# Performance work log

Hardware: AMD Instinct MI355X
Metric: run time of the kernel (lower is better)

The kernel has to match this reference:

```python
import jax, jax.numpy as jnp
import numpy as np

H, W = 256, 512
SCORE_THR = 0.2
NMS_THR = 0.15
TOPK = 4096


def _make_anchors():
    xs = (np.arange(W) + 0.5) * 0.4 - 0.2 * W
    ys = (np.arange(H) + 0.5) * 0.4 - 0.2 * H
    gx, gy = np.meshgrid(xs, ys)            # [H, W]
    anc = np.zeros((H, W, 2, 7), dtype=np.float32)
    anc[..., 0] = gx[..., None]
    anc[..., 1] = gy[..., None]
    anc[..., 2] = -1.0
    anc[..., 3] = 1.56  # h
    anc[..., 4] = 1.6   # w
    anc[..., 5] = 3.9   # l
    anc[..., 0, 6] = 0.0
    anc[..., 1, 6] = np.pi / 2
    return jnp.asarray(anc)


def _make_T(theta, tx, ty, tz):
    c, s = np.cos(theta), np.sin(theta)
    T = np.eye(4, dtype=np.float32)
    T[0, 0], T[0, 1], T[1, 0], T[1, 1] = c, -s, s, c
    T[0, 3], T[1, 3], T[2, 3] = tx, ty, tz
    return jnp.asarray(T)


def setup_inputs() -> dict:
    key = jax.random.key(0)
    k1, k2, k3, k4 = jax.random.split(key, 4)
    return {
        "anchors": _make_anchors(),
        "psm_v": jax.random.normal(k1, (1, 2, H, W), jnp.float32),
        "rm_v": jax.random.normal(k2, (1, 14, H, W), jnp.float32) * 0.1,
        "psm_i": jax.random.normal(k3, (1, 2, H, W), jnp.float32),
        "rm_i": jax.random.normal(k4, (1, 14, H, W), jnp.float32) * 0.1,
        "t_proj": _make_T(0.05, 2.0, -1.0, 0.1),
        "t_ego": _make_T(-0.1, 5.0, 3.0, 0.0),
    }


def delta_to_boxes3d(rm, anchors):
    # rm: [1, 14, H, W] -> [A, 7]; anchors: [H, W, 2, 7] xyzhwlr -> [A, 7]
    d = jnp.transpose(rm[0], (1, 2, 0)).reshape(-1, 7)
    a = anchors.reshape(-1, 7)
    ad = jnp.sqrt(a[:, 4] ** 2 + a[:, 5] ** 2)          # diag of w,l
    xy = d[:, :2] * ad[:, None] + a[:, :2]
    z = d[:, 2] * a[:, 3] + a[:, 2]
    dims = jnp.exp(d[:, 3:6]) * a[:, 3:6]               # h, w, l
    yaw = d[:, 6] + a[:, 6]
    return jnp.concatenate([xy, z[:, None], dims, yaw[:, None]], axis=1)


def boxes_to_corners_3d(b):
    # b: [N, 7] x,y,z,h,w,l,yaw (order 'hwl') -> [N, 8, 3]
    h, w, l, yaw = b[:, 3], b[:, 4], b[:, 5], b[:, 6]
    sx = jnp.array([1, 1, -1, -1, 1, 1, -1, -1], jnp.float32) * 0.5
    sy = jnp.array([1, -1, -1, 1, 1, -1, -1, 1], jnp.float32) * 0.5
    sz = jnp.array([-1, -1, -1, -1, 1, 1, 1, 1], jnp.float32) * 0.5
    x = l[:, None] * sx
    y = w[:, None] * sy
    z = h[:, None] * sz
    c, s = jnp.cos(yaw)[:, None], jnp.sin(yaw)[:, None]
    xr = x * c - y * s + b[:, 0:1]
    yr = x * s + y * c + b[:, 1:2]
    zr = z + b[:, 2:3]
    return jnp.stack([xr, yr, zr], axis=-1)


def project_box3d(corners, T):
    # corners: [N, 8, 3]; T: [4, 4]
    return jnp.einsum('ij,nkj->nki', T[:3, :3], corners) + T[:3, 3]


def corner_to_center(corners):
    # inverse of boxes_to_corners_3d, order 'hwl'
    xyz = corners.mean(axis=1)
    h = corners[:, 4:, 2].mean(axis=1) - corners[:, :4, 2].mean(axis=1)
    dl = corners[:, (0, 1, 4, 5), :2] - corners[:, (3, 2, 7, 6), :2]
    dw = corners[:, (0, 3, 4, 7), :2] - corners[:, (1, 2, 5, 6), :2]
    l = jnp.linalg.norm(dl, axis=-1).mean(axis=1)
    w = jnp.linalg.norm(dw, axis=-1).mean(axis=1)
    d = dl.sum(axis=1)
    yaw = jnp.arctan2(d[:, 1], d[:, 0])
    return jnp.concatenate(
        [xyz, h[:, None], w[:, None], l[:, None], yaw[:, None]], axis=1)


def standup_boxes(corners):
    # [N, 8, 3] -> [N, 4] x1,y1,x2,y2 over BEV
    mn = corners[..., :2].min(axis=1)
    mx = corners[..., :2].max(axis=1)
    return jnp.concatenate([mn, mx], axis=1)


def iou_matrix(b):
    area = (b[:, 2] - b[:, 0]) * (b[:, 3] - b[:, 1])
    lt = jnp.maximum(b[:, None, :2], b[None, :, :2])
    rb = jnp.minimum(b[:, None, 2:], b[None, :, 2:])
    wh = jnp.clip(rb - lt, 0.0)
    inter = wh[..., 0] * wh[..., 1]
    return inter / (area[:, None] + area[None, :] - inter + 1e-6)


def nms_keep(iou, valid, thresh):
    K = iou.shape[0]
    idx = jnp.arange(K)

    def body(i, keep):
        sup = (iou[i] > thresh) & (idx > i) & keep[i]
        return keep & ~sup

    return jax.lax.fori_loop(0, K, body, valid)


def _branch(psm, rm, anchors):
    scores = jax.nn.sigmoid(jnp.transpose(psm[0], (1, 2, 0))).reshape(-1)
    boxes = delta_to_boxes3d(rm, anchors)
    return boxes, scores


def reference(anchors, psm_v, rm_v, psm_i, rm_i, t_proj, t_ego):
    boxes_v, scores_v = _branch(psm_v, rm_v, anchors)
    boxes_i, scores_i = _branch(psm_i, rm_i, anchors)
    # project infra branch boxes into ego frame via corner transform
    corners_i = boxes_to_corners_3d(boxes_i)
    boxes_i = corner_to_center(project_box3d(corners_i, t_proj))
    boxes = jnp.concatenate([boxes_v, boxes_i], axis=0)       # [2A, 7]
    scores = jnp.concatenate([scores_v, scores_i], axis=0)    # [2A]
    # project all to ego space
    proj = project_box3d(boxes_to_corners_3d(boxes), t_ego)   # [2A, 8, 3]
    # static replacement of masked_select: mask + top-K
    masked = jnp.where(scores > SCORE_THR, scores, -1.0)
    top_s, top_i = jax.lax.top_k(masked, TOPK)
    corners_k = proj[top_i]                                    # [K, 8, 3]
    iou = iou_matrix(standup_boxes(corners_k))
    keep = nms_keep(iou, top_s > SCORE_THR, NMS_THR)
    final = top_s * keep.astype(top_s.dtype)
    # pack corners + surviving scores: [K, 25]
    return jnp.concatenate([corners_k.reshape(TOPK, 24), final[:, None]], axis=1)
```

## Files before the change

kernel.cpp:

```cpp
#include <hip/hip_runtime.h>
#include <stdint.h>

typedef unsigned int u32;
typedef unsigned long long u64;

#define HH 256
#define WW 512
#define HW (HH*WW)
#define N2 (2*HW)
#define NT (2*N2)
#define TOPK 4096
#define SCORE_THR 0.2f
#define NMS_THR 0.15f

#define OFF_KEYS   0ull
#define OFF_GHIST  ((size_t)NT*4)
#define OFF_GHIST2 (OFF_GHIST + 4096)
#define OFF_CNT    (OFF_GHIST2 + 4096)
#define OFF_VALIDM (OFF_CNT + 16)
#define OFF_CAND   (OFF_VALIDM + 512)
#define OFF_STAND  OFF_CAND
#define OFF_SELIDX (OFF_CAND + 65536)
#define OFF_SELSC  (OFF_SELIDX + (size_t)TOPK*4)
#define OFF_TDIAG  (OFF_SELSC + (size_t)TOPK*4)
#define ZERO_BYTES (4096 + 4096 + 16)
#define RANK_J 8

#define NMSW 4
#define RPW 16
#define WREG_U64 1088
#define SLOT_U64 (NMSW * WREG_U64)

__device__ __forceinline__ u32 f2ord(float f) {
    u32 b = __float_as_uint(f);
    return (b & 0x80000000u) ? ~b : (b | 0x80000000u);
}

__global__ void __launch_bounds__(1024) k_keys(const float* __restrict__ psm_v,
                                               const float* __restrict__ psm_i,
                                               u32* __restrict__ keys,
                                               u32* __restrict__ ghist) {
    __shared__ u32 lh[1024];
    int t = threadIdx.x;
    lh[t] = 0;
    __syncthreads();
    int n = blockIdx.x * 1024 + t;
    int br = n >> 18;
    int m  = n & (N2 - 1);
    int a  = m & 1;
    int hw = m >> 1;
    const float* psm = br ? psm_i : psm_v;
    float x = psm[a * HW + hw];
    float s = 1.0f / (1.0f + __builtin_expf(-x));
    u32 key = 0u;
    if (s > SCORE_THR) key = f2ord(s);
    keys[n] = key;
    if (key) atomicAdd(&lh[key >> 22], 1u);
    __syncthreads();
    u32 c = lh[t];
    if (c) atomicAdd(&ghist[t], c);
}

__device__ __forceinline__ void pivot1024(const u32* __restrict__ arr, u32 target,
                                          u32* out_bin, u32* out_next, int l) {
    u32 h[16], loc[16];
#pragma unroll
    for (int j = 0; j < 16; ++j) h[j] = arr[l * 16 + j];
    loc[15] = h[15];
#pragma unroll
    for (int j = 14; j >= 0; --j) loc[j] = loc[j + 1] + h[j];
    u32 T = loc[0];
    u32 incl = T;
#pragma unroll
    for (int d = 1; d < 64; d <<= 1) {
        u32 v = __shfl_down(incl, d);
        if (l + d < 64) incl += v;
    }
    u32 E = incl - T;
#pragma unroll
    for (int j = 0; j < 16; ++j) {
        u32 S  = loc[j] + E;
        u32 Sn = (j < 15 ? loc[j + 1] : 0u) + E;
        if (S >= target && Sn < target) {
            *out_bin = (u32)(l * 16 + j);
            *out_next = Sn;
        }
    }
}

__global__ void __launch_bounds__(1024) k_hist2(const u32* __restrict__ ghist,
                                                const u32* __restrict__ keys,
                                                u32* __restrict__ ghist2) {
    __shared__ u32 lh[1024];
    __shared__ u32 b1_sh;
    int tid = threadIdx.x;
    lh[tid] = 0;
    if (tid < 64) {
        u32 bin = 0xFFFFFFFFu, nxt = 0;
        pivot1024(ghist, (u32)TOPK, &bin, &nxt, tid);
        if (bin != 0xFFFFFFFFu) b1_sh = bin;
    }
    __syncthreads();
    u32 b1 = b1_sh;
    int n = blockIdx.x * 1024 + tid;
    u32 key = keys[n];
    if ((key >> 22) == b1) atomicAdd(&lh[(key >> 12) & 1023u], 1u);
    __syncthreads();
    u32 c = lh[tid];
    if (c) atomicAdd(&ghist2[tid], c);
}

__global__ void __launch_bounds__(1024) k_collect(const u32* __restrict__ ghist,
                                                  const u32* __restrict__ ghist2,
                                                  const u32* __restrict__ keys,
                                                  u64* __restrict__ cand,
                                                  u32* __restrict__ cnt) {
    __shared__ u32 b1_sh, t2_sh, b2_sh;
    int tid = threadIdx.x;
    if (tid < 64) {
        u32 bin = 0xFFFFFFFFu, nxt = 0;
        pivot1024(ghist, (u32)TOPK, &bin, &nxt, tid);
        if (bin != 0xFFFFFFFFu) { b1_sh = bin; t2_sh = (u32)TOPK - nxt; }
    }
    __syncthreads();
    if (tid < 64) {
        u32 bin = 0xFFFFFFFFu, nxt = 0;
        pivot1024(ghist2, t2_sh, &bin, &nxt, tid);
        if (bin != 0xFFFFFFFFu) b2_sh = bin;
    }
    __syncthreads();
    u32 thr20 = (b1_sh << 10) | b2_sh;
    int n = blockIdx.x * 1024 + tid;
    u32 key = keys[n];
    if ((key >> 12) >= thr20) {
        u32 pos = atomicAdd(cnt, 1u);
        if (pos < 8192u)
            cand[pos] = ((u64)key << 32) | (u64)(u32)(~(u32)n);
    }
}

__global__ void __launch_bounds__(256) k_rank1(const u64* __restrict__ cand,
                                               const u32* __restrict__ cnt,
                                               u32* __restrict__ partial) {
    __shared__ u64 tile[1024];
    int tid = threadIdx.x;
    int i = blockIdx.x * 256 + tid;
    u32 base = blockIdx.y * 1024u;
    u32 c = *cnt;
    if (c > 8192u) c = 8192u;
    u64 my = (i < (int)c) ? cand[i] : 0ull;
#pragma unroll
    for (int k = 0; k < 4; ++k) {
        u32 idx = base + tid + k * 256;
        tile[tid + k * 256] = (idx < c) ? cand[idx] : 0ull;
    }
    __syncthreads();
    u32 lim = (c > base) ? ((c - base < 1024u) ? (c - base) : 1024u) : 0u;
    u32 r = 0;
#pragma unroll 4
    for (u32 k = 0; k < lim; ++k) r += (tile[k] > my) ? 1u : 0u;
    partial[blockIdx.y * 8192 + i] = r;
}

__global__ void __launch_bounds__(256) k_scatter(const u64* __restrict__ cand,
                                                 const u32* __restrict__ cnt,
                                                 const u32* __restrict__ partial,
                                                 u32* __restrict__ sel_idx) {
    int i = blockIdx.x * 256 + threadIdx.x;
    u32 c = *cnt;
    if (c > 8192u) c = 8192u;
    if (i >= (int)c) return;
    u32 rank = 0;
#pragma unroll
    for (int bj = 0; bj < RANK_J; ++bj) rank += partial[bj * 8192 + i];
    if (rank < (u32)TOPK) {
        u64 my = cand[i];
        sel_idx[rank] = ~((u32)(my & 0xFFFFFFFFull));
    }
}

__device__ __forceinline__ void box_corners(const float b[7], float cx[8], float cy[8], float cz[8]) {
    const float sx[8] = {0.5f,0.5f,-0.5f,-0.5f,0.5f,0.5f,-0.5f,-0.5f};
    const float sy[8] = {0.5f,-0.5f,-0.5f,0.5f,0.5f,-0.5f,-0.5f,0.5f};
    const float sz[8] = {-0.5f,-0.5f,-0.5f,-0.5f,0.5f,0.5f,0.5f,0.5f};
    float c = __builtin_cosf(b[6]), s = __builtin_sinf(b[6]);
#pragma unroll
    for (int k = 0; k < 8; k++) {
        float x = b[5] * sx[k], y = b[4] * sy[k], z = b[3] * sz[k];
        cx[k] = x * c - y * s + b[0];
        cy[k] = x * s + y * c + b[1];
        cz[k] = z + b[2];
    }
}

__device__ __forceinline__ void proj_T(const float* __restrict__ T, float cx[8], float cy[8], float cz[8]) {
#pragma unroll
    for (int k = 0; k < 8; k++) {
        float x = cx[k], y = cy[k], z = cz[k];
        cx[k] = T[0] * x + T[1] * y + T[2]  * z + T[3];
        cy[k] = T[4] * x + T[5] * y + T[6]  * z + T[7];
        cz[k] = T[8] * x + T[9] * y + T[10] * z + T[11];
    }
}

__device__ __forceinline__ void corner_to_center(const float cx[8], const float cy[8], const float cz[8], float b[7]) {
    float mx = 0.f, my = 0.f, mz = 0.f;
#pragma unroll
    for (int k = 0; k < 8; k++) { mx += cx[k]; my += cy[k]; mz += cz[k]; }
    mx *= 0.125f; my *= 0.125f; mz *= 0.125f;
    float htop = (cz[4] + cz[5] + cz[6] + cz[7]) * 0.25f;
    float hbot = (cz[0] + cz[1] + cz[2] + cz[3]) * 0.25f;
    const int lA[4] = {0,1,4,5}, lB[4] = {3,2,7,6};
    const int wA[4] = {0,3,4,7}, wB[4] = {1,2,5,6};
    float l = 0.f, w = 0.f, dx = 0.f, dy = 0.f;
#pragma unroll
    for (int i = 0; i < 4; i++) {
        float ax = cx[lA[i]] - cx[lB[i]];
        float ay = cy[lA[i]] - cy[lB[i]];
        l += __builtin_sqrtf(ax * ax + ay * ay);
        dx += ax; dy += ay;
    }
#pragma unroll
    for (int i = 0; i < 4; i++) {
        float ax = cx[wA[i]] - cx[wB[i]];
        float ay = cy[wA[i]] - cy[wB[i]];
        w += __builtin_sqrtf(ax * ax + ay * ay);
    }
    b[0] = mx; b[1] = my; b[2] = mz;
    b[3] = htop - hbot;
    b[4] = w * 0.25f;
    b[5] = l * 0.25f;
    b[6] = atan2f(dy, dx);
}

__global__ void __launch_bounds__(256) k_boxes(const float* __restrict__ anchors,
                                               const float* __restrict__ psm_v,
                                               const float* __restrict__ psm_i,
                                               const float* __restrict__ rm_v,
                                               const float* __restrict__ rm_i,
                                               const float* __restrict__ tproj,
                                               const float* __restrict__ tego,
                                               const u32* __restrict__ sel_idx,
                                               float* __restrict__ sel_sc,
                                               float* __restrict__ out,
                                               float4* __restrict__ stand,
                                               u64* __restrict__ validm) {
    int k = blockIdx.x * blockDim.x + threadIdx.x;
    if (k >= TOPK) return;
    int n = (int)(sel_idx[k] & (u32)(NT - 1));
    int br = n >> 18;
    int m  = n & (N2 - 1);
    int a  = m & 1;
    int hw = m >> 1;

    const float* psm = br ? psm_i : psm_v;
    float xs = psm[a * HW + hw];
    float s  = 1.0f / (1.0f + __builtin_expf(-xs));
    sel_sc[k] = (s > SCORE_THR) ? s : -1.0f;
    u64 vbits = __ballot(s > SCORE_THR);
    if ((threadIdx.x & 63) == 0) validm[k >> 6] = vbits;

    const float* rm = br ? rm_i : rm_v;
    float d[7];
#pragma unroll
    for (int j = 0; j < 7; j++) d[j] = rm[(a * 7 + j) * HW + hw];
    const float* anc = anchors + (size_t)m * 7;
    float a0 = anc[0], a1 = anc[1], a2 = anc[2], a3 = anc[3], a4 = anc[4], a5 = anc[5], a6 = anc[6];
    float ad = __builtin_sqrtf(a4 * a4 + a5 * a5);
    float b[7];
    b[0] = d[0] * ad + a0;
    b[1] = d[1] * ad + a1;
    b[2] = d[2] * a3 + a2;
    b[3] = __builtin_expf(d[3]) * a3;
    b[4] = __builtin_expf(d[4]) * a4;
    b[5] = __builtin_expf(d[5]) * a5;
    b[6] = d[6] + a6;

    if (br) {
        float cx[8], cy[8], cz[8];
        box_corners(b, cx, cy, cz);
        proj_T(tproj, cx, cy, cz);
        corner_to_center(cx, cy, cz, b);
    }

    float cx[8], cy[8], cz[8];
    box_corners(b, cx, cy, cz);
    proj_T(tego, cx, cy, cz);

    float mnx = cx[0], mny = cy[0], mxx = cx[0], mxy = cy[0];
#pragma unroll
    for (int c = 0; c < 8; c++) {
        out[(size_t)k * 25 + c * 3 + 0] = cx[c];
        out[(size_t)k * 25 + c * 3 + 1] = cy[c];
        out[(size_t)k * 25 + c * 3 + 2] = cz[c];
        mnx = fminf(mnx, cx[c]); mny = fminf(mny, cy[c]);
        mxx = fmaxf(mxx, cx[c]); mxy = fmaxf(mxy, cy[c]);
    }
    stand[k] = make_float4(mnx, mny, mxx, mxy);
}

__global__ void __launch_bounds__(256) k_mask(const float4* __restrict__ stand,
                                              u64* __restrict__ mask) {
    int i = blockIdx.x * 4 + (threadIdx.x >> 6);
    int t = threadIdx.x & 63;
    int w0 = i >> 6;
    float4 bi = stand[i];
    float areai = (bi.z - bi.x) * (bi.w - bi.y);
    u64 myword = 0ull;
    for (int w = w0; w < 64; ++w) {
        int j = w * 64 + t;
        float4 bj = stand[j];
        float areaj = (bj.z - bj.x) * (bj.w - bj.y);
        float ltx = fmaxf(bi.x, bj.x), lty = fmaxf(bi.y, bj.y);
        float rbx = fminf(bi.z, bj.z), rby = fminf(bi.w, bj.w);
        float iw = fmaxf(rbx - ltx, 0.0f), ih = fmaxf(rby - lty, 0.0f);
        float inter = iw * ih;
        float iou = inter / (areai + areaj - inter + 1e-6f);
        bool sup = (iou > NMS_THR) && (j > i);
        u64 bits = __ballot(sup);
        if (t == w) myword = bits;
    }
    mask[(size_t)i * 64 + t] = myword;
}

__global__ void __launch_bounds__(64) k_diag(const float4* __restrict__ stand,
                                             u64* __restrict__ tdiag) {
    __shared__ float4 sb[64];
    int B = blockIdx.x, l = threadIdx.x;
    float4 me = stand[B * 64 + l];
    sb[l] = me;
    __syncthreads();
    float aream = (me.z - me.x) * (me.w - me.y);
    u64 T = 0ull;
    for (int j = 0; j < 64; ++j) {
        float4 bj = sb[j];
        float areaj = (bj.z - bj.x) * (bj.w - bj.y);
        float ltx = fmaxf(bj.x, me.x), lty = fmaxf(bj.y, me.y);
        float rbx = fminf(bj.z, me.z), rby = fminf(bj.w, me.w);
        float iw = fmaxf(rbx - ltx, 0.0f), ih = fmaxf(rby - lty, 0.0f);
        float inter = iw * ih;
        float iou = inter / (areaj + aream - inter + 1e-6f);
        bool sup = (iou > NMS_THR) && (j < l);
        T |= sup ? (1ull << j) : 0ull;
    }
    tdiag[B * 64 + l] = T;
}

__device__ __forceinline__ u64 readlane64(u64 v, int lane) {
    u32 lo = (u32)__builtin_amdgcn_readlane((int)(u32)v, lane);
    u32 hi = (u32)__builtin_amdgcn_readlane((int)(u32)(v >> 32), lane);
    return ((u64)hi << 32) | (u64)lo;
}

__device__ __forceinline__ void nms_stage(const u64* __restrict__ mask,
                                          const u64* __restrict__ tdiag,
                                          int c, int s, int sw, int l,
                                          u64* ring) {
    u64* wb = ring + (size_t)s * SLOT_U64 + (size_t)sw * WREG_U64;
    bool act = (2 * (l & 31) + 1) >= c;
    const u64* gb = mask + (size_t)c * 4096 + (size_t)(sw * RPW) * 64 + (size_t)l * 2;
    if (act) {
#pragma unroll
        for (int k = 0; k < 8; ++k) {
            __builtin_amdgcn_global_load_lds(
                (const __attribute__((address_space(1))) void*)(gb + k * 128),
                (__attribute__((address_space(3))) void*)(wb + k * 128), 16, 0, 0);
        }
    }
    if (l < 32) {
        __builtin_amdgcn_global_load_lds(
            (const __attribute__((address_space(1))) void*)(tdiag + (size_t)c * 64 + (size_t)l * 2),
            (__attribute__((address_space(3))) void*)(wb + 1024), 16, 0, 0);
    }
}

__global__ void __launch_bounds__(NMSW * 64, 1)
k_nms(const u64* __restrict__ mask,
      const u64* __restrict__ tdiag,
      const u64* __restrict__ validm,
      const float* __restrict__ sc,
      float* __restrict__ out) {
    __shared__ u64 ring[3 * SLOT_U64];
    __shared__ u64 sh[2 * NMSW];
    int l  = threadIdx.x & 63;
    int sw = __builtin_amdgcn_readfirstlane((int)(threadIdx.x >> 6));
    u64 remv = 0ull;
    u64 keep = 0ull;
    u64 vreg = validm[l];

    nms_stage(mask, tdiag, 0, 0, sw, l, ring);
    nms_stage(mask, tdiag, 1, 1, sw, l, ring);
    nms_stage(mask, tdiag, 2, 2, sw, l, ring);

    for (int B = 0; B < 64; ++B) {
        int s = B % 3;
        u64* wb = ring + (size_t)s * SLOT_U64 + (size_t)sw * WREG_U64;
        u64 x = readlane64(remv, B);
        if (l == 0) sh[(B & 1) * NMSW + sw] = x;
        __asm__ volatile("" ::: "memory");
        __builtin_amdgcn_s_waitcnt(0xC07F);
        __builtin_amdgcn_s_barrier();
        __asm__ volatile("" ::: "memory");
        __builtin_amdgcn_s_waitcnt(0x4F72);
        __builtin_amdgcn_sched_barrier(0);
        __asm__ volatile("" ::: "memory");
        const volatile u64* sp = sh + (B & 1) * NMSW;
        u64 curw = sp[0] | sp[1] | sp[2] | sp[3];
        u64 Tl = wb[1024 + l];
        u64 row[RPW];
#pragma unroll
        for (int k = 0; k < RPW; ++k) row[k] = wb[(size_t)k * 64 + l];
        u64 vm = readlane64(vreg, B);
        u64 ve = vm & ~curw;
        u64 D = 0ull, P = ve;
        while (D != P) {
            u64 nD = ve & ~__ballot((Tl & P) != 0ull);
            u64 nP = ve & ~__ballot((Tl & nD) != 0ull);
            D = nD; P = nP;
        }
        u64 kb = D;
        keep = (l == B) ? kb : keep;
        u64 kbw = (kb >> (sw * RPW)) & 0xFFFFull;
        u64 p = 0ull;
#pragma unroll
        for (int k = 0; k < RPW; ++k)
            p |= row[k] & (0ull - ((kbw >> k) & 1ull));
        remv |= p;
        if (B + 3 < 64) nms_stage(mask, tdiag, B + 3, s, sw, l, ring);
    }

    for (int k = 0; k < RPW; ++k) {
        int c = sw * RPW + k;
        u64 kc = readlane64(keep, c);
        float s = sc[c * 64 + l];
        out[(size_t)(c * 64 + l) * 25 + 24] = ((kc >> l) & 1ull) ? s : 0.0f;
    }
}

extern "C" void kernel_launch(void* const* d_in, const int* in_sizes, int n_in,
                              void* d_out, int out_size, void* d_ws, size_t ws_size,
                              hipStream_t stream) {
    const float* anchors = (const float*)d_in[0];
    const float* psm_v   = (const float*)d_in[1];
    const float* rm_v    = (const float*)d_in[2];
    const float* psm_i   = (const float*)d_in[3];
    const float* rm_i    = (const float*)d_in[4];
    const float* tproj   = (const float*)d_in[5];
    const float* tego    = (const float*)d_in[6];
    float* out = (float*)d_out;
    char* ws = (char*)d_ws;

    u32*    keys    = (u32*)(ws + OFF_KEYS);
    u64*    mask    = (u64*)(ws + OFF_KEYS);
    u32*    partial = (u32*)(ws + OFF_KEYS);
    u32*    ghist   = (u32*)(ws + OFF_GHIST);
    u32*    ghist2  = (u32*)(ws + OFF_GHIST2);
    u32*    cnt     = (u32*)(ws + OFF_CNT);
    u64*    validm  = (u64*)(ws + OFF_VALIDM);
    u64*    cand    = (u64*)(ws + OFF_CAND);
    float4* stand   = (float4*)(ws + OFF_STAND);
    u32*    sel_idx = (u32*)(ws + OFF_SELIDX);
    float*  sel_sc  = (float*)(ws + OFF_SELSC);
    u64*    tdiag   = (u64*)(ws + OFF_TDIAG);

    hipMemsetAsync(ws + OFF_GHIST, 0, ZERO_BYTES, stream);
    k_keys   <<<NT / 1024, 1024, 0, stream>>>(psm_v, psm_i, keys, ghist);
    k_hist2  <<<NT / 1024, 1024, 0, stream>>>(ghist, keys, ghist2);
    k_collect<<<NT / 1024, 1024, 0, stream>>>(ghist, ghist2, keys, cand, cnt);
    k_rank1  <<<dim3(32, RANK_J), 256, 0, stream>>>(cand, cnt, partial);
    k_scatter<<<32, 256, 0, stream>>>(cand, cnt, partial, sel_idx);
    k_boxes  <<<TOPK / 256, 256, 0, stream>>>(anchors, psm_v, psm_i, rm_v, rm_i,
                                              tproj, tego, sel_idx, sel_sc, out,
                                              stand, validm);
    k_mask   <<<TOPK / 4, 256, 0, stream>>>(stand, mask);
    k_diag   <<<64, 64, 0, stream>>>(stand, tdiag);
    k_nms    <<<1, NMSW * 64, 0, stream>>>(mask, tdiag, validm, sel_sc, out);
}
```

Measured before the change: 244.1 us.

## Fuse scatter into rank, merge mask/diag kernels, software-pipeline NMS row loads

```diff
diff --git a/kernel.cpp b/kernel.cpp
--- a/kernel.cpp
+++ b/kernel.cpp
@@ -141,8 +141,11 @@
 
 __global__ void __launch_bounds__(256) k_rank1(const u64* __restrict__ cand,
                                                const u32* __restrict__ cnt,
-                                               u32* __restrict__ partial) {
+                                               u32* __restrict__ partial,
+                                               u32* __restrict__ done,
+                                               u32* __restrict__ sel_idx) {
     __shared__ u64 tile[1024];
+    __shared__ u32 lastsh;
     int tid = threadIdx.x;
     int i = blockIdx.x * 256 + tid;
     u32 base = blockIdx.y * 1024u;
@@ -160,22 +163,20 @@
 #pragma unroll 4
     for (u32 k = 0; k < lim; ++k) r += (tile[k] > my) ? 1u : 0u;
     partial[blockIdx.y * 8192 + i] = r;
-}
-
-__global__ void __launch_bounds__(256) k_scatter(const u64* __restrict__ cand,
-                                                 const u32* __restrict__ cnt,
-                                                 const u32* __restrict__ partial,
-                                                 u32* __restrict__ sel_idx) {
-    int i = blockIdx.x * 256 + threadIdx.x;
-    u32 c = *cnt;
-    if (c > 8192u) c = 8192u;
-    if (i >= (int)c) return;
-    u32 rank = 0;
-#pragma unroll
-    for (int bj = 0; bj < RANK_J; ++bj) rank += partial[bj * 8192 + i];
-    if (rank < (u32)TOPK) {
-        u64 my = cand[i];
-        sel_idx[rank] = ~((u32)(my & 0xFFFFFFFFull));
+    __threadfence();
+    __syncthreads();
+    if (tid == 0)
+        lastsh = (atomicAdd(done, 1u) == (u32)(32 * RANK_J - 1)) ? 1u : 0u;
+    __syncthreads();
+    if (lastsh) {
+        __threadfence();
+        for (u32 it = tid; it < c; it += 256u) {
+            u32 rank = 0;
+#pragma unroll
+            for (int bj = 0; bj < RANK_J; ++bj) rank += partial[bj * 8192 + it];
+            if (rank < (u32)TOPK)
+                sel_idx[rank] = ~((u32)(cand[it] & 0xFFFFFFFFull));
+        }
     }
 }
 
@@ -233,18 +234,18 @@
     b[6] = atan2f(dy, dx);
 }
 
-__global__ void __launch_bounds__(256) k_boxes(const float* __restrict__ anchors,
-                                               const float* __restrict__ psm_v,
-                                               const float* __restrict__ psm_i,
-                                               const float* __restrict__ rm_v,
-                                               const float* __restrict__ rm_i,
-                                               const float* __restrict__ tproj,
-                                               const float* __restrict__ tego,
-                                               const u32* __restrict__ sel_idx,
-                                               float* __restrict__ sel_sc,
-                                               float* __restrict__ out,
-                                               float4* __restrict__ stand,
-                                               u64* __restrict__ validm) {
+__global__ void __launch_bounds__(64) k_boxes(const float* __restrict__ anchors,
+                                              const float* __restrict__ psm_v,
+                                              const float* __restrict__ psm_i,
+                                              const float* __restrict__ rm_v,
+                                              const float* __restrict__ rm_i,
+                                              const float* __restrict__ tproj,
+                                              const float* __restrict__ tego,
+                                              const u32* __restrict__ sel_idx,
+                                              float* __restrict__ sel_sc,
+                                              float* __restrict__ out,
+                                              float4* __restrict__ stand,
+                                              u64* __restrict__ validm) {
     int k = blockIdx.x * blockDim.x + threadIdx.x;
     if (k >= TOPK) return;
     int n = (int)(sel_idx[k] & (u32)(NT - 1));
@@ -299,51 +300,54 @@
     stand[k] = make_float4(mnx, mny, mxx, mxy);
 }
 
-__global__ void __launch_bounds__(256) k_mask(const float4* __restrict__ stand,
-                                              u64* __restrict__ mask) {
-    int i = blockIdx.x * 4 + (threadIdx.x >> 6);
-    int t = threadIdx.x & 63;
-    int w0 = i >> 6;
-    float4 bi = stand[i];
-    float areai = (bi.z - bi.x) * (bi.w - bi.y);
-    u64 myword = 0ull;
-    for (int w = w0; w < 64; ++w) {
-        int j = w * 64 + t;
-        float4 bj = stand[j];
-        float areaj = (bj.z - bj.x) * (bj.w - bj.y);
-        float ltx = fmaxf(bi.x, bj.x), lty = fmaxf(bi.y, bj.y);
-        float rbx = fminf(bi.z, bj.z), rby = fminf(bi.w, bj.w);
-        float iw = fmaxf(rbx - ltx, 0.0f), ih = fmaxf(rby - lty, 0.0f);
-        float inter = iw * ih;
-        float iou = inter / (areai + areaj - inter + 1e-6f);
-        bool sup = (iou > NMS_THR) && (j > i);
-        u64 bits = __ballot(sup);
-        if (t == w) myword = bits;
-    }
-    mask[(size_t)i * 64 + t] = myword;
-}
-
-__global__ void __launch_bounds__(64) k_diag(const float4* __restrict__ stand,
-                                             u64* __restrict__ tdiag) {
-    __shared__ float4 sb[64];
-    int B = blockIdx.x, l = threadIdx.x;
-    float4 me = stand[B * 64 + l];
-    sb[l] = me;
-    __syncthreads();
-    float aream = (me.z - me.x) * (me.w - me.y);
-    u64 T = 0ull;
-    for (int j = 0; j < 64; ++j) {
-        float4 bj = sb[j];
-        float areaj = (bj.z - bj.x) * (bj.w - bj.y);
-        float ltx = fmaxf(bj.x, me.x), lty = fmaxf(bj.y, me.y);
-        float rbx = fminf(bj.z, me.z), rby = fminf(bj.w, me.w);
-        float iw = fmaxf(rbx - ltx, 0.0f), ih = fmaxf(rby - lty, 0.0f);
-        float inter = iw * ih;
-        float iou = inter / (areaj + aream - inter + 1e-6f);
-        bool sup = (iou > NMS_THR) && (j < l);
-        T |= sup ? (1ull << j) : 0ull;
-    }
-    tdiag[B * 64 + l] = T;
+__global__ void __launch_bounds__(256) k_maskdiag(const float4* __restrict__ stand,
+                                                  u64* __restrict__ mask,
+                                                  u64* __restrict__ tdiag) {
+    __shared__ float4 sb[256];
+    int bid = blockIdx.x;
+    if (bid < 1024) {
+        int i = bid * 4 + (threadIdx.x >> 6);
+        int t = threadIdx.x & 63;
+        int w0 = i >> 6;
+        float4 bi = stand[i];
+        float areai = (bi.z - bi.x) * (bi.w - bi.y);
+        u64 myword = 0ull;
+        for (int w = w0; w < 64; ++w) {
+            int j = w * 64 + t;
+            float4 bj = stand[j];
+            float areaj = (bj.z - bj.x) * (bj.w - bj.y);
+            float ltx = fmaxf(bi.x, bj.x), lty = fmaxf(bi.y, bj.y);
+            float rbx = fminf(bi.z, bj.z), rby = fminf(bi.w, bj.w);
+            float iw = fmaxf(rbx - ltx, 0.0f), ih = fmaxf(rby - lty, 0.0f);
+            float inter = iw * ih;
+            float iou = inter / (areai + areaj - inter + 1e-6f);
+            bool sup = (iou > NMS_THR) && (j > i);
+            u64 bits = __ballot(sup);
+            if (t == w) myword = bits;
+        }
+        mask[(size_t)i * 64 + t] = myword;
+    } else {
+        int d = bid - 1024;
+        int tid = threadIdx.x;
+        sb[tid] = stand[d * 256 + tid];
+        __syncthreads();
+        int sub = tid >> 6, l = tid & 63;
+        float4 me = sb[sub * 64 + l];
+        float aream = (me.z - me.x) * (me.w - me.y);
+        u64 T = 0ull;
+        for (int j = 0; j < 64; ++j) {
+            float4 bj = sb[sub * 64 + j];
+            float areaj = (bj.z - bj.x) * (bj.w - bj.y);
+            float ltx = fmaxf(bj.x, me.x), lty = fmaxf(bj.y, me.y);
+            float rbx = fminf(bj.z, me.z), rby = fminf(bj.w, me.w);
+            float iw = fmaxf(rbx - ltx, 0.0f), ih = fmaxf(rby - lty, 0.0f);
+            float inter = iw * ih;
+            float iou = inter / (areaj + aream - inter + 1e-6f);
+            bool sup = (iou > NMS_THR) && (j < l);
+            T |= sup ? (1ull << j) : 0ull;
+        }
+        tdiag[(size_t)(d * 4 + sub) * 64 + l] = T;
+    }
 }
 
 __device__ __forceinline__ u64 readlane64(u64 v, int lane) {
@@ -354,17 +358,15 @@
 
 __device__ __forceinline__ void nms_stage(const u64* __restrict__ mask,
                                           const u64* __restrict__ tdiag,
-                                          int c, int s, int sw, int l,
-                                          u64* ring) {
-    u64* wb = ring + (size_t)s * SLOT_U64 + (size_t)sw * WREG_U64;
+                                          int c, int sw, int l, u64* wb) {
     bool act = (2 * (l & 31) + 1) >= c;
     const u64* gb = mask + (size_t)c * 4096 + (size_t)(sw * RPW) * 64 + (size_t)l * 2;
     if (act) {
 #pragma unroll
         for (int k = 0; k < 8; ++k) {
             __builtin_amdgcn_global_load_lds(
-                (const __attribute__((address_space(1))) void*)(gb + k * 128),
-                (__attribute__((address_space(3))) void*)(wb + k * 128), 16, 0, 0);
+                (const __attribute__((address_space(1))) void*)(gb + (size_t)k * 128),
+                (__attribute__((address_space(3))) void*)(wb + (size_t)k * 128), 16, 0, 0);
         }
     }
     if (l < 32) {
@@ -372,6 +374,55 @@
             (const __attribute__((address_space(1))) void*)(tdiag + (size_t)c * 64 + (size_t)l * 2),
             (__attribute__((address_space(3))) void*)(wb + 1024), 16, 0, 0);
     }
+}
+
+__device__ __forceinline__ void nms_ldrows(const u64* wb, int l,
+                                           u64 (&rows)[RPW], u64& Tl) {
+    Tl = wb[1024 + l];
+#pragma unroll
+    for (int k = 0; k < RPW; ++k) rows[k] = wb[(size_t)k * 64 + l];
+}
+
+template<int VMC, bool REFILL, bool PRELOAD>
+__device__ __forceinline__ void nms_chunk(int B, int l, int sw,
+                                          const u64 (&rows)[RPW], u64 Tl,
+                                          u64 (&nrows)[RPW], u64& nTl,
+                                          u64* wb_cur, u64* wb_next,
+                                          u64 vreg, volatile u64* sh,
+                                          u64& remv, u64& keep,
+                                          const u64* __restrict__ mask,
+                                          const u64* __restrict__ tdiag) {
+    u64 x = readlane64(remv, B);
+    if (l == 0) sh[(B & 1) * NMSW + sw] = x;
+    __asm__ volatile("" ::: "memory");
+    __builtin_amdgcn_s_waitcnt(0xC07F);
+    __builtin_amdgcn_s_barrier();
+    __asm__ volatile("" ::: "memory");
+    if constexpr (VMC == 9) __builtin_amdgcn_s_waitcnt(0x0F79);
+    else if constexpr (VMC == 0) __builtin_amdgcn_s_waitcnt(0x0F70);
+    __builtin_amdgcn_sched_barrier(0);
+    __asm__ volatile("" ::: "memory");
+    if constexpr (REFILL) nms_stage(mask, tdiag, B + 3, sw, l, wb_cur);
+    if constexpr (PRELOAD) nms_ldrows(wb_next, l, nrows, nTl);
+    __builtin_amdgcn_sched_barrier(0);
+    const volatile u64* sp = sh + (B & 1) * NMSW;
+    u64 curw = sp[0] | sp[1] | sp[2] | sp[3];
+    u64 vm = readlane64(vreg, B);
+    u64 ve = vm & ~curw;
+    u64 D = 0ull, P = ve;
+    while (D != P) {
+        u64 nD = ve & ~__ballot((Tl & P) != 0ull);
+        u64 nP = ve & ~__ballot((Tl & nD) != 0ull);
+        D = nD; P = nP;
+    }
+    u64 kb = D;
+    keep = (l == B) ? kb : keep;
+    u64 kbw = (kb >> (sw * RPW)) & 0xFFFFull;
+    u64 p = 0ull;
+#pragma unroll
+    for (int k = 0; k < RPW; ++k)
+        p |= rows[k] & (0ull - ((kbw >> k) & 1ull));
+    remv |= p;
 }
 
 __global__ void __launch_bounds__(NMSW * 64, 1)
@@ -388,45 +439,46 @@
     u64 keep = 0ull;
     u64 vreg = validm[l];
 
-    nms_stage(mask, tdiag, 0, 0, sw, l, ring);
-    nms_stage(mask, tdiag, 1, 1, sw, l, ring);
-    nms_stage(mask, tdiag, 2, 2, sw, l, ring);
-
-    for (int B = 0; B < 64; ++B) {
-        int s = B % 3;
-        u64* wb = ring + (size_t)s * SLOT_U64 + (size_t)sw * WREG_U64;
-        u64 x = readlane64(remv, B);
-        if (l == 0) sh[(B & 1) * NMSW + sw] = x;
-        __asm__ volatile("" ::: "memory");
-        __builtin_amdgcn_s_waitcnt(0xC07F);
-        __builtin_amdgcn_s_barrier();
-        __asm__ volatile("" ::: "memory");
-        __builtin_amdgcn_s_waitcnt(0x4F72);
-        __builtin_amdgcn_sched_barrier(0);
-        __asm__ volatile("" ::: "memory");
-        const volatile u64* sp = sh + (B & 1) * NMSW;
-        u64 curw = sp[0] | sp[1] | sp[2] | sp[3];
-        u64 Tl = wb[1024 + l];
-        u64 row[RPW];
-#pragma unroll
-        for (int k = 0; k < RPW; ++k) row[k] = wb[(size_t)k * 64 + l];
-        u64 vm = readlane64(vreg, B);
-        u64 ve = vm & ~curw;
-        u64 D = 0ull, P = ve;
-        while (D != P) {
-            u64 nD = ve & ~__ballot((Tl & P) != 0ull);
-            u64 nP = ve & ~__ballot((Tl & nD) != 0ull);
-            D = nD; P = nP;
-        }
-        u64 kb = D;
-        keep = (l == B) ? kb : keep;
-        u64 kbw = (kb >> (sw * RPW)) & 0xFFFFull;
-        u64 p = 0ull;
-#pragma unroll
-        for (int k = 0; k < RPW; ++k)
-            p |= row[k] & (0ull - ((kbw >> k) & 1ull));
-        remv |= p;
-        if (B + 3 < 64) nms_stage(mask, tdiag, B + 3, s, sw, l, ring);
+    u64* wbs0 = ring + 0 * SLOT_U64 + (size_t)sw * WREG_U64;
+    u64* wbs1 = ring + 1 * SLOT_U64 + (size_t)sw * WREG_U64;
+    u64* wbs2 = ring + 2 * SLOT_U64 + (size_t)sw * WREG_U64;
+    nms_stage(mask, tdiag, 0, sw, l, wbs0);
+    nms_stage(mask, tdiag, 1, sw, l, wbs1);
+    nms_stage(mask, tdiag, 2, sw, l, wbs2);
+    __builtin_amdgcn_s_waitcnt(0x4F72);
+    __builtin_amdgcn_sched_barrier(0);
+    __asm__ volatile("" ::: "memory");
+    u64 rowA[RPW], rowB[RPW], TlA, TlB;
+    nms_ldrows(wbs0, l, rowA, TlA);
+
+    int sA = 0;
+    for (int B = 0; B < 60; B += 2) {
+        int s1 = sA + 1; if (s1 == 3) s1 = 0;
+        int s2 = s1 + 1; if (s2 == 3) s2 = 0;
+        u64* wbA = ring + (size_t)sA * SLOT_U64 + (size_t)sw * WREG_U64;
+        u64* wbB = ring + (size_t)s1 * SLOT_U64 + (size_t)sw * WREG_U64;
+        u64* wbC = ring + (size_t)s2 * SLOT_U64 + (size_t)sw * WREG_U64;
+        nms_chunk<9, true, true>(B,     l, sw, rowA, TlA, rowB, TlB, wbA, wbB,
+                                 vreg, sh, remv, keep, mask, tdiag);
+        nms_chunk<9, true, true>(B + 1, l, sw, rowB, TlB, rowA, TlA, wbB, wbC,
+                                 vreg, sh, remv, keep, mask, tdiag);
+        sA = s2;
+    }
+    {
+        int s1 = sA + 1; if (s1 == 3) s1 = 0;
+        int s2 = s1 + 1; if (s2 == 3) s2 = 0;
+        u64* wb60 = ring + (size_t)sA * SLOT_U64 + (size_t)sw * WREG_U64;
+        u64* wb61 = ring + (size_t)s1 * SLOT_U64 + (size_t)sw * WREG_U64;
+        u64* wb62 = ring + (size_t)s2 * SLOT_U64 + (size_t)sw * WREG_U64;
+        u64* wb63 = wb60;
+        nms_chunk<9,  true,  true >(60, l, sw, rowA, TlA, rowB, TlB, wb60, wb61,
+                                    vreg, sh, remv, keep, mask, tdiag);
+        nms_chunk<9,  false, true >(61, l, sw, rowB, TlB, rowA, TlA, wb61, wb62,
+                                    vreg, sh, remv, keep, mask, tdiag);
+        nms_chunk<0,  false, true >(62, l, sw, rowA, TlA, rowB, TlB, wb62, wb63,
+                                    vreg, sh, remv, keep, mask, tdiag);
+        nms_chunk<-1, false, false>(63, l, sw, rowB, TlB, rowA, TlA, wb63, wb63,
+                                    vreg, sh, remv, keep, mask, tdiag);
     }
 
     for (int k = 0; k < RPW; ++k) {
@@ -456,6 +508,7 @@
     u32*    ghist   = (u32*)(ws + OFF_GHIST);
     u32*    ghist2  = (u32*)(ws + OFF_GHIST2);
     u32*    cnt     = (u32*)(ws + OFF_CNT);
+    u32*    done    = (u32*)(ws + OFF_CNT + 4);
     u64*    validm  = (u64*)(ws + OFF_VALIDM);
     u64*    cand    = (u64*)(ws + OFF_CAND);
     float4* stand   = (float4*)(ws + OFF_STAND);
@@ -464,15 +517,13 @@
     u64*    tdiag   = (u64*)(ws + OFF_TDIAG);
 
     hipMemsetAsync(ws + OFF_GHIST, 0, ZERO_BYTES, stream);
-    k_keys   <<<NT / 1024, 1024, 0, stream>>>(psm_v, psm_i, keys, ghist);
-    k_hist2  <<<NT / 1024, 1024, 0, stream>>>(ghist, keys, ghist2);
-    k_collect<<<NT / 1024, 1024, 0, stream>>>(ghist, ghist2, keys, cand, cnt);
-    k_rank1  <<<dim3(32, RANK_J), 256, 0, stream>>>(cand, cnt, partial);
-    k_scatter<<<32, 256, 0, stream>>>(cand, cnt, partial, sel_idx);
-    k_boxes  <<<TOPK / 256, 256, 0, stream>>>(anchors, psm_v, psm_i, rm_v, rm_i,
-                                              tproj, tego, sel_idx, sel_sc, out,
-                                              stand, validm);
-    k_mask   <<<TOPK / 4, 256, 0, stream>>>(stand, mask);
-    k_diag   <<<64, 64, 0, stream>>>(stand, tdiag);
-    k_nms    <<<1, NMSW * 64, 0, stream>>>(mask, tdiag, validm, sel_sc, out);
-}
+    k_keys    <<<NT / 1024, 1024, 0, stream>>>(psm_v, psm_i, keys, ghist);
+    k_hist2   <<<NT / 1024, 1024, 0, stream>>>(ghist, keys, ghist2);
+    k_collect <<<NT / 1024, 1024, 0, stream>>>(ghist, ghist2, keys, cand, cnt);
+    k_rank1   <<<dim3(32, RANK_J), 256, 0, stream>>>(cand, cnt, partial, done, sel_idx);
+    k_boxes   <<<TOPK / 64, 64, 0, stream>>>(anchors, psm_v, psm_i, rm_v, rm_i,
+                                             tproj, tego, sel_idx, sel_sc, out,
+                                             stand, validm);
+    k_maskdiag<<<1040, 256, 0, stream>>>(stand, mask, tdiag);
+    k_nms     <<<1, NMSW * 64, 0, stream>>>(mask, tdiag, validm, sel_sc, out);
+}
```

Measured after the change: 269.1 us. 1.1x slower.
